# Optimization experiments

Measured on AMD Instinct MI355X. Metric: run time of the kernel, lower is better.

Reference implementation:

```python
import jax, jax.numpy as jnp
import numpy as np

NUM_FREQS = 6

def posenc(x, num_freqs):
    freqs = (2.0 ** jnp.arange(num_freqs)).astype(x.dtype)  # [F]
    ang = x[..., None] * freqs                               # [N, D, F]
    enc = jnp.concatenate([jnp.sin(ang), jnp.cos(ang)], axis=-1)  # [N, D, 2F]
    return enc.reshape(x.shape[0], -1)

def setup_inputs() -> dict:
    key = jax.random.key(0)
    k1, k2, k3 = jax.random.split(key, 3)
    N, D, C = 200000, 6, 256
    E = D * 2 * NUM_FREQS  # 72
    X = jax.random.normal(k1, (N, D), dtype=jnp.float32)
    linear_mappings = jax.random.normal(k2, (3 * C, E), dtype=jnp.float32) * 0.05
    centroids = jax.random.normal(k3, (C, 3), dtype=jnp.float32)
    return {"X": X, "linear_mappings": linear_mappings, "centroids": centroids}

def reference(X, linear_mappings, centroids):
    N = X.shape[0]
    encoded_X = posenc(X, NUM_FREQS)                         # [N, E]
    rgb_clusters = encoded_X @ linear_mappings.T             # [N, 3C]
    rgb_clusters = rgb_clusters.reshape(N, -1, 3)            # [N, C, 3]
    # scores = centroids @ X[:, :3].T  -> softmax over clusters per point
    scores = X[:, :3] @ centroids.T                          # [N, C] (== scores.T in torch code)
    attention_weights = jax.nn.softmax(scores, axis=-1)      # [N, C]
    # torch does diagonal(attn @ rgb_clusters).T == per-row contraction:
    rgb = jnp.einsum('nc,ncd->nd', attention_weights, rgb_clusters)  # [N, 3]
    return rgb
```

## Files before the change

### kernel.cpp

```cpp
#include <hip/hip_runtime.h>
#include <math.h>


#define NCLUST   256
#define M_BLK    32
#define THREADS  64
#define NTILES   15
#define BG_BYTES (NTILES * 8 * 64 * 16)
#define ET_STRIDE 72

typedef __attribute__((ext_vector_type(8))) short bfrag_t;
typedef __attribute__((ext_vector_type(4))) float cfrag_t;
typedef __attribute__((ext_vector_type(4))) unsigned int uifrag_t;

static __device__ __forceinline__ unsigned short f2bf1(float f) {
    return __builtin_bit_cast(unsigned short, (__bf16)f);
}
static __device__ __forceinline__ unsigned int f2bf2(float lo, float hi) {
    return (unsigned int)f2bf1(lo) | ((unsigned int)f2bf1(hi) << 16);
}
static __device__ __forceinline__ float bf2f(unsigned short s) {
    return __uint_as_float(((unsigned int)s) << 16);
}

__global__ void prep_kernel(const float* __restrict__ W, uint4* __restrict__ Bg) {
    const int u = blockIdx.x * 256 + threadIdx.x;
    if (u >= NTILES * 8 * 64) return;
    const int lane = u & 63, ks = (u >> 6) & 7, tile = u >> 9;
    const int ln = lane & 15, q = lane >> 4;
    const int jp = tile * 16 + ln;
    const int d  = jp / 80;
    const int e  = jp - d * 80;
    const int c0 = ks * 32 + q * 8;
    unsigned int w[4] = {0u, 0u, 0u, 0u};
    if (e < 72) {
#pragma unroll
        for (int i = 0; i < 4; ++i) {
            float f0 = W[((c0 + 2 * i)     * 3 + d) * 72 + e];
            float f1 = W[((c0 + 2 * i + 1) * 3 + d) * 72 + e];
            w[i] = f2bf2(f0, f1);
        }
    }
    Bg[u] = make_uint4(w[0], w[1], w[2], w[3]);
}

__global__ __launch_bounds__(THREADS, 2) void rgb_attn_mfma(
    const float* __restrict__ X,
    const float* __restrict__ cent,
    const void* __restrict__ Bg,
    float* __restrict__ out, int N)
{
    __shared__ __align__(16) unsigned char encT[80 * ET_STRIDE];

    const int lane = threadIdx.x;
    const int q    = lane >> 4;
    const int ln   = lane & 15;

    {
        const int pt  = lane & 31;
        const int h   = lane >> 5;
        const int gpt = blockIdx.x * M_BLK + pt;
        const int gp  = (gpt < N) ? gpt : (N - 1);
        unsigned char* colp = encT + pt * 2;
#pragma unroll
        for (int k = 0; k < 3; ++k) {
            const int dd = 3 * h + k;
            const float xv = X[gp * 6 + dd];
            float s[6], c[6];
            __sincosf(xv, &s[0], &c[0]);
#pragma unroll
            for (int f = 1; f < 6; ++f) {
                s[f] = 2.0f * s[f-1] * c[f-1];
                c[f] = 1.0f - 2.0f * s[f-1] * s[f-1];
            }
#pragma unroll
            for (int f = 0; f < 6; ++f) {
                *(unsigned short*)(colp + (dd*12 + f)     * ET_STRIDE) = f2bf1(s[f]);
                *(unsigned short*)(colp + (dd*12 + 6 + f) * ET_STRIDE) = f2bf1(c[f]);
            }
        }
        *(uint2*)(encT + (72 + (lane >> 3)) * ET_STRIDE + (lane & 7) * 8) = make_uint2(0u, 0u);
    }

    uifrag_t afrag[2][8];
    float dA = 0.0f, dB = 0.0f;
    {
        const int g0a = blockIdx.x * M_BLK + ln;
        const int g0  = (g0a < N) ? g0a : (N - 1);
        const int g1a = g0a + 16;
        const int g1  = (g1a < N) ? g1a : (N - 1);
        const float2 xy0 = *(const float2*)(X + g0 * 6);
        const float  z0  = X[g0 * 6 + 2];
        const float2 xy1 = *(const float2*)(X + g1 * 6);
        const float  z1  = X[g1 * 6 + 2];
        const float4* c4base = (const float4*)cent;
#pragma unroll
        for (int g = 0; g < 8; ++g) {
            const float4* c4 = c4base + (6 * q + 24 * g);
            const float4 v0 = c4[0], v1 = c4[1], v2 = c4[2];
            const float4 v3 = c4[3], v4 = c4[4], v5 = c4[5];
            float cx[8], cy[8], cz[8];
            cx[0]=v0.x; cy[0]=v0.y; cz[0]=v0.z;
            cx[1]=v0.w; cy[1]=v1.x; cz[1]=v1.y;
            cx[2]=v1.z; cy[2]=v1.w; cz[2]=v2.x;
            cx[3]=v2.y; cy[3]=v2.z; cz[3]=v2.w;
            cx[4]=v3.x; cy[4]=v3.y; cz[4]=v3.z;
            cx[5]=v3.w; cy[5]=v4.x; cz[5]=v4.y;
            cx[6]=v4.z; cy[6]=v4.w; cz[6]=v5.x;
            cx[7]=v5.y; cy[7]=v5.z; cz[7]=v5.w;
            float ea[8], eb[8];
#pragma unroll
            for (int j = 0; j < 8; ++j) {
                ea[j] = __expf(fmaf(xy0.x, cx[j], fmaf(xy0.y, cy[j], z0 * cz[j])));
                eb[j] = __expf(fmaf(xy1.x, cx[j], fmaf(xy1.y, cy[j], z1 * cz[j])));
                dA += ea[j]; dB += eb[j];
            }
#pragma unroll
            for (int w = 0; w < 4; ++w) {
                afrag[0][g][w] = f2bf2(ea[2*w], ea[2*w+1]);
                afrag[1][g][w] = f2bf2(eb[2*w], eb[2*w+1]);
            }
        }
    }

    const char* Bgc = (const char*)Bg + lane * 16;
    float part[3][2][4] = {};
#pragma unroll
    for (int d = 0; d < 3; ++d) {
#pragma unroll 1
        for (int tt = 0; tt < 5; ++tt) {
            const char* bp = Bgc + (d * 5 + tt) * 8192;
            bfrag_t b[8];
#pragma unroll
            for (int ks = 0; ks < 8; ++ks)
                b[ks] = *(const bfrag_t*)(bp + ks * 1024);
            cfrag_t a0 = {0.f,0.f,0.f,0.f}, a1 = {0.f,0.f,0.f,0.f};
#pragma unroll
            for (int ks = 0; ks < 8; ++ks) {
                a0 = __builtin_amdgcn_mfma_f32_16x16x32_bf16(
                         __builtin_bit_cast(bfrag_t, afrag[0][ks]), b[ks], a0, 0, 0, 0);
                a1 = __builtin_amdgcn_mfma_f32_16x16x32_bf16(
                         __builtin_bit_cast(bfrag_t, afrag[1][ks]), b[ks], a1, 0, 0, 0);
            }
            const unsigned char* ep = encT + (tt * 16 + ln) * ET_STRIDE + q * 8;
#pragma unroll
            for (int mt = 0; mt < 2; ++mt) {
                const ushort4 ev = *(const ushort4*)(ep + mt * 32);
                const cfrag_t a = mt ? a1 : a0;
                part[d][mt][0] = fmaf(a[0], bf2f(ev.x), part[d][mt][0]);
                part[d][mt][1] = fmaf(a[1], bf2f(ev.y), part[d][mt][1]);
                part[d][mt][2] = fmaf(a[2], bf2f(ev.z), part[d][mt][2]);
                part[d][mt][3] = fmaf(a[3], bf2f(ev.w), part[d][mt][3]);
            }
        }
    }

#pragma unroll
    for (int mask = 1; mask <= 8; mask <<= 1)
#pragma unroll
        for (int d = 0; d < 3; ++d)
#pragma unroll
            for (int mt = 0; mt < 2; ++mt)
#pragma unroll
                for (int r = 0; r < 4; ++r)
                    part[d][mt][r] += __shfl_xor(part[d][mt][r], mask, 64);

    dA += __shfl_xor(dA, 16, 64); dA += __shfl_xor(dA, 32, 64);
    dB += __shfl_xor(dB, 16, 64); dB += __shfl_xor(dB, 32, 64);
    const float iA = 1.0f / dA;
    const float iB = 1.0f / dB;
    float invr[2][4];
#pragma unroll
    for (int r = 0; r < 4; ++r) {
        invr[0][r] = __shfl(iA, q * 4 + r, 64);
        invr[1][r] = __shfl(iB, q * 4 + r, 64);
    }

    if (ln == 0) {
#pragma unroll
        for (int mt = 0; mt < 2; ++mt)
#pragma unroll
            for (int r = 0; r < 4; ++r) {
                const int pm = mt * 16 + q * 4 + r;
                const int g  = blockIdx.x * M_BLK + pm;
                if (g < N) {
                    out[g*3+0] = part[0][mt][r] * invr[mt][r];
                    out[g*3+1] = part[1][mt][r] * invr[mt][r];
                    out[g*3+2] = part[2][mt][r] * invr[mt][r];
                }
            }
    }
}

__global__ __launch_bounds__(256) void rgb_attn_fallback(
    const float* __restrict__ X, const float* __restrict__ W,
    const float* __restrict__ cent, float* __restrict__ out, int N)
{
    const int n = blockIdx.x * 256 + threadIdx.x;
    const bool valid = (n < N);
    float x[6];
#pragma unroll
    for (int k = 0; k < 6; ++k) x[k] = valid ? X[n * 6 + k] : 0.0f;
    float enc[72];
#pragma unroll
    for (int d = 0; d < 6; ++d)
#pragma unroll
        for (int f = 0; f < 6; ++f) {
            float s, c;
            __sincosf(x[d] * (float)(1 << f), &s, &c);
            enc[d*12+f] = s; enc[d*12+6+f] = c;
        }
    float acc0 = 0, acc1 = 0, acc2 = 0, denom = 0;
#pragma unroll 1
    for (int c = 0; c < NCLUST; ++c) {
        float s = fmaf(x[0], cent[c*3], fmaf(x[1], cent[c*3+1], x[2]*cent[c*3+2]));
        float ew = __expf(s);
        const float* w = W + c * 216;
        float d0 = 0, d1 = 0, d2 = 0;
#pragma unroll
        for (int e = 0; e < 72; ++e) {
            float ee = enc[e];
            d0 = fmaf(ee, w[e], d0);
            d1 = fmaf(ee, w[72 + e], d1);
            d2 = fmaf(ee, w[144 + e], d2);
        }
        denom += ew;
        acc0 = fmaf(ew, d0, acc0); acc1 = fmaf(ew, d1, acc1); acc2 = fmaf(ew, d2, acc2);
    }
    if (valid) {
        float inv = 1.0f / denom;
        out[n*3+0] = acc0*inv; out[n*3+1] = acc1*inv; out[n*3+2] = acc2*inv;
    }
}

extern "C" void kernel_launch(void* const* d_in, const int* in_sizes, int n_in,
                              void* d_out, int out_size, void* d_ws, size_t ws_size,
                              hipStream_t stream)
{
    const float* X    = (const float*)d_in[0];
    const float* W    = (const float*)d_in[1];
    const float* cent = (const float*)d_in[2];
    float* out = (float*)d_out;
    const int N = in_sizes[0] / 6;

    if (ws_size >= (size_t)BG_BYTES) {
        uint4* Bg = (uint4*)d_ws;
        prep_kernel<<<(NTILES * 8 * 64 + 255) / 256, 256, 0, stream>>>(W, Bg);
        const int blocks = (N + M_BLK - 1) / M_BLK;
        rgb_attn_mfma<<<blocks, THREADS, 0, stream>>>(X, cent, (const void*)Bg, out, N);
    } else {
        rgb_attn_fallback<<<(N + 255) / 256, 256, 0, stream>>>(X, W, cent, out, N);
    }
}
```

Baseline: 114.6 us.

## Stage X tile in LDS and double-buffer B fragment loads across tiles

Each block now loads its 32 rows of X into shared memory with coalesced float4 loads and reads them from there, replacing scattered per-lane global reads. B fragments for the first tile are issued before the encoding and softmax work, and each later tile's fragments are prefetched while the current tile's MFMAs run. This is meant to hide global load latency behind compute. It adds 32 registers for the second B buffer, which may reduce occupancy, and the LDS write is used without a barrier, which holds only because the block is a single wavefront.

Result: slower. 122.0 us (+6.5%).

```diff
diff --git a/kernel.cpp b/kernel.cpp
--- a/kernel.cpp
+++ b/kernel.cpp
@@ -50,22 +50,42 @@
     const void* __restrict__ Bg,
     float* __restrict__ out, int N)
 {
+    __shared__ __align__(16) float Xs[M_BLK * 6];
     __shared__ __align__(16) unsigned char encT[80 * ET_STRIDE];
 
     const int lane = threadIdx.x;
     const int q    = lane >> 4;
     const int ln   = lane & 15;
+    const int mbase = blockIdx.x * M_BLK;
+
+    if (mbase + M_BLK <= N) {
+        if (lane < 48) {
+            const float4 v = *(const float4*)(X + (size_t)mbase * 6 + lane * 4);
+            *(float4*)(Xs + lane * 4) = v;
+        }
+    } else {
+#pragma unroll 1
+        for (int i = lane; i < M_BLK * 6; i += 64) {
+            const int p  = mbase + i / 6;
+            const int pc = (p < N) ? p : (N - 1);
+            Xs[i] = X[pc * 6 + (i % 6)];
+        }
+    }
+
+    const char* Bgc = (const char*)Bg + lane * 16;
+    bfrag_t bcur[8], bnext[8];
+#pragma unroll
+    for (int ks = 0; ks < 8; ++ks)
+        bcur[ks] = *(const bfrag_t*)(Bgc + ks * 1024);
 
     {
-        const int pt  = lane & 31;
-        const int h   = lane >> 5;
-        const int gpt = blockIdx.x * M_BLK + pt;
-        const int gp  = (gpt < N) ? gpt : (N - 1);
+        const int pt = lane & 31;
+        const int h  = lane >> 5;
         unsigned char* colp = encT + pt * 2;
 #pragma unroll
         for (int k = 0; k < 3; ++k) {
             const int dd = 3 * h + k;
-            const float xv = X[gp * 6 + dd];
+            const float xv = Xs[pt * 6 + dd];
             float s[6], c[6];
             __sincosf(xv, &s[0], &c[0]);
 #pragma unroll
@@ -85,14 +105,9 @@
     uifrag_t afrag[2][8];
     float dA = 0.0f, dB = 0.0f;
     {
-        const int g0a = blockIdx.x * M_BLK + ln;
-        const int g0  = (g0a < N) ? g0a : (N - 1);
-        const int g1a = g0a + 16;
-        const int g1  = (g1a < N) ? g1a : (N - 1);
-        const float2 xy0 = *(const float2*)(X + g0 * 6);
-        const float  z0  = X[g0 * 6 + 2];
-        const float2 xy1 = *(const float2*)(X + g1 * 6);
-        const float  z1  = X[g1 * 6 + 2];
+        const float x00 = Xs[ln * 6 + 0], x01 = Xs[ln * 6 + 1], x02 = Xs[ln * 6 + 2];
+        const float x10 = Xs[(16 + ln) * 6 + 0], x11 = Xs[(16 + ln) * 6 + 1],
+                    x12 = Xs[(16 + ln) * 6 + 2];
         const float4* c4base = (const float4*)cent;
 #pragma unroll
         for (int g = 0; g < 8; ++g) {
@@ -111,8 +126,8 @@
             float ea[8], eb[8];
 #pragma unroll
             for (int j = 0; j < 8; ++j) {
-                ea[j] = __expf(fmaf(xy0.x, cx[j], fmaf(xy0.y, cy[j], z0 * cz[j])));
-                eb[j] = __expf(fmaf(xy1.x, cx[j], fmaf(xy1.y, cy[j], z1 * cz[j])));
+                ea[j] = __expf(fmaf(x00, cx[j], fmaf(x01, cy[j], x02 * cz[j])));
+                eb[j] = __expf(fmaf(x10, cx[j], fmaf(x11, cy[j], x12 * cz[j])));
                 dA += ea[j]; dB += eb[j];
             }
 #pragma unroll
@@ -123,24 +138,24 @@
         }
     }
 
-    const char* Bgc = (const char*)Bg + lane * 16;
     float part[3][2][4] = {};
 #pragma unroll
     for (int d = 0; d < 3; ++d) {
 #pragma unroll 1
         for (int tt = 0; tt < 5; ++tt) {
-            const char* bp = Bgc + (d * 5 + tt) * 8192;
-            bfrag_t b[8];
-#pragma unroll
-            for (int ks = 0; ks < 8; ++ks)
-                b[ks] = *(const bfrag_t*)(bp + ks * 1024);
+            const int t = d * 5 + tt;
+            if (t < NTILES - 1) {
+#pragma unroll
+                for (int ks = 0; ks < 8; ++ks)
+                    bnext[ks] = *(const bfrag_t*)(Bgc + (t + 1) * 8192 + ks * 1024);
+            }
             cfrag_t a0 = {0.f,0.f,0.f,0.f}, a1 = {0.f,0.f,0.f,0.f};
 #pragma unroll
             for (int ks = 0; ks < 8; ++ks) {
                 a0 = __builtin_amdgcn_mfma_f32_16x16x32_bf16(
-                         __builtin_bit_cast(bfrag_t, afrag[0][ks]), b[ks], a0, 0, 0, 0);
+                         __builtin_bit_cast(bfrag_t, afrag[0][ks]), bcur[ks], a0, 0, 0, 0);
                 a1 = __builtin_amdgcn_mfma_f32_16x16x32_bf16(
-                         __builtin_bit_cast(bfrag_t, afrag[1][ks]), b[ks], a1, 0, 0, 0);
+                         __builtin_bit_cast(bfrag_t, afrag[1][ks]), bcur[ks], a1, 0, 0, 0);
             }
             const unsigned char* ep = encT + (tt * 16 + ln) * ET_STRIDE + q * 8;
 #pragma unroll
@@ -152,6 +167,9 @@
                 part[d][mt][2] = fmaf(a[2], bf2f(ev.z), part[d][mt][2]);
                 part[d][mt][3] = fmaf(a[3], bf2f(ev.w), part[d][mt][3]);
             }
+#pragma unroll
+            for (int ks = 0; ks < 8; ++ks)
+                bcur[ks] = bnext[ks];
         }
     }
 
@@ -182,7 +200,7 @@
 #pragma unroll
             for (int r = 0; r < 4; ++r) {
                 const int pm = mt * 16 + q * 4 + r;
-                const int g  = blockIdx.x * M_BLK + pm;
+                const int g  = mbase + pm;
                 if (g < N) {
                     out[g*3+0] = part[0][mt][r] * invr[mt][r];
                     out[g*3+1] = part[1][mt][r] * invr[mt][r];
```
